# Kernel optimization log

Hardware: AMD Instinct MI355X
Metric: run time of the kernel (lower is better)

The kernel has to match this reference:

```python
import jax, jax.numpy as jnp
import numpy as np

N = 25600   # total nodes
B = 256     # graphs / batch_size / LSTM seq length
F = 128     # num_feat
H = 256     # gnn_hidden
R = 512     # rnn_hidden == 2*H (forced by alm layer)
L = 2       # rnn_layers
V = 32000   # vocab
E = 409600  # edges
NPG = 100   # nodes per graph (forced by alm layer / attention reshape)


def setup_inputs() -> dict:
    key = jax.random.key(0)
    ks = jax.random.split(key, 20)
    def rn(k, shape, fan_in, scale=1.0):
        return jax.random.normal(k, shape, jnp.float32) * (scale / np.sqrt(fan_in))
    inp = {}
    inp['x'] = jax.random.normal(ks[0], (N, F), jnp.float32)
    inp['edge_index'] = jax.random.randint(ks[1], (2, E), 0, N)
    inp['bwd_edge_index'] = jnp.flip(inp['edge_index'], axis=0)
    inp['batch'] = jnp.arange(N) // NPG  # contiguous graphs, 100 nodes each
    inp['h0'] = jax.random.normal(ks[2], (L, 1, R), jnp.float32)
    inp['c0'] = jax.random.normal(ks[3], (L, 1, R), jnp.float32)
    inp['W_gnn'] = rn(ks[4], (F, H), F)
    inp['W_root'] = rn(ks[5], (H, H), H)
    inp['W_nbr'] = rn(ks[6], (H, H), H)
    inp['b_conv'] = jnp.zeros((H,), jnp.float32)
    D = 2 * H
    inp['W1'] = rn(ks[7], (D, D), D); inp['b1'] = jnp.zeros((D,), jnp.float32)
    inp['gamma'] = jnp.ones((D,), jnp.float32); inp['beta'] = jnp.zeros((D,), jnp.float32)
    inp['W2'] = rn(ks[8], (D, D), D); inp['b2'] = jnp.zeros((D,), jnp.float32)
    A = NPG * R + R  # alm input dim = rnn_hidden*100 + rnn_hidden
    inp['W_alm'] = rn(ks[9], (NPG, A), A, scale=0.1)
    inp['b_alm'] = jnp.ones((NPG,), jnp.float32)  # keeps alpha.sum() well away from 0
    inp['Wih0'] = rn(ks[10], (4 * R, D), D); inp['Whh0'] = rn(ks[11], (4 * R, R), R)
    inp['bih0'] = jnp.zeros((4 * R,), jnp.float32); inp['bhh0'] = jnp.zeros((4 * R,), jnp.float32)
    inp['Wih1'] = rn(ks[12], (4 * R, R), R); inp['Whh1'] = rn(ks[13], (4 * R, R), R)
    inp['bih1'] = jnp.zeros((4 * R,), jnp.float32); inp['bhh1'] = jnp.zeros((4 * R,), jnp.float32)
    inp['W_fc'] = rn(ks[14], (R, V), R); inp['b_fc'] = jnp.zeros((V,), jnp.float32)
    return inp


def _lstm_layer(inputs, h, c, Wih, Whh, bih, bhh):
    # inputs: (T, 1, in); carry h, c: (1, R). PyTorch gate order i, f, g, o.
    def step(carry, xt):
        h, c = carry
        g = xt @ Wih.T + bih + h @ Whh.T + bhh
        i, f, gg, o = jnp.split(g, 4, axis=-1)
        c = jax.nn.sigmoid(f) * c + jax.nn.sigmoid(i) * jnp.tanh(gg)
        h = jax.nn.sigmoid(o) * jnp.tanh(c)
        return (h, c), h
    (hT, cT), outs = jax.lax.scan(step, (h, c), inputs)
    return outs, hT, cT


def reference(x, edge_index, bwd_edge_index, batch, h0, c0, W_gnn, W_root, W_nbr, b_conv,
              W1, b1, gamma, beta, W2, b2, W_alm, b_alm,
              Wih0, Whh0, bih0, bhh0, Wih1, Whh1, bih1, bhh1, W_fc, b_fc):
    n = x.shape[0]
    x = x @ W_gnn  # (N, H)
    # GraphConv: out_i = W_root x_i + W_nbr * sum_{j->i} x_j + b.
    # (Original loops gnn_layers times from the SAME x, so only the last conv matters.)
    def conv(xx, ei):
        agg = jax.ops.segment_sum(xx[ei[0]], ei[1], num_segments=n)
        return xx @ W_root + agg @ W_nbr + b_conv
    fwd_x = jax.nn.relu(conv(x, edge_index))
    bwd_x = jax.nn.relu(conv(x, bwd_edge_index))
    xc = jnp.concatenate([fwd_x, bwd_x], axis=1)  # (N, 2H) == (N, R)
    # MLP [2H, 2H, 2H]: Lin -> BatchNorm(batch stats) -> ReLU -> (dropout off) -> Lin
    h1 = xc @ W1 + b1
    h1 = (h1 - h1.mean(0)) / jnp.sqrt(h1.var(0) + 1e-5) * gamma + beta
    x_mlp = jax.nn.relu(h1) @ W2 + b2
    # global mean pool over graphs
    counts = jax.ops.segment_sum(jnp.ones((n,), x_mlp.dtype), batch, num_segments=B)
    x_g = jax.ops.segment_sum(x_mlp, batch, num_segments=B) / counts[:, None]
    x_emb = x_g.reshape(B, 1, 2 * H)  # LSTM: seq_len=B, batch=1
    # attention over cell state (vectorized form of the nested loops):
    # alpha[l,b,:] = alm(cat(c0[l].flatten(), h3[b].flatten())); normalize by sum (NOT softmax);
    # new_c[l] = sum_b alpha[l,b,:] @ h3[b]
    h3 = xc.reshape(B, NPG, R)
    s = c0.reshape(L, R)
    Ws, Wh = W_alm[:, :R], W_alm[:, R:]
    alpha = (s @ Ws.T)[:, None, :] + (h3.reshape(B, NPG * R) @ Wh.T)[None] + b_alm  # (L,B,NPG)
    alpha = alpha / alpha.sum(-1, keepdims=True)
    new_c = jnp.einsum('lbk,bkd->ld', alpha, h3)  # (L, R)
    # 2-layer LSTM (eval mode: inter-layer dropout is identity)
    outs, hT0, cT0 = _lstm_layer(x_emb, h0[0], new_c[0:1], Wih0, Whh0, bih0, bhh0)
    outs, hT1, cT1 = _lstm_layer(outs, h0[1], new_c[1:2], Wih1, Whh1, bih1, bhh1)
    preds = (outs @ W_fc + b_fc)[:, -1, :]  # (B, V)
    return preds
```

## Files before the change

kernel.cpp:

```cpp
#include <hip/hip_runtime.h>
#include <math.h>

#define N_NODES 25600
#define F_IN    128
#define H_GNN   256
#define D_MLP   512
#define E_EDGE  409600
#define B_GR    256
#define NPG_    100
#define R_LSTM  512
#define V_OUT   32000

typedef __bf16 bf16x8 __attribute__((ext_vector_type(8)));
typedef float  f32x4  __attribute__((ext_vector_type(4)));
typedef unsigned short u16x8 __attribute__((ext_vector_type(8)));

__device__ __forceinline__ unsigned short f2bf(float x) {
    unsigned u = __builtin_bit_cast(unsigned, x);
    unsigned r = (u + 0x7FFFu + ((u >> 16) & 1u)) >> 16;
    return (unsigned short)r;
}

template<bool TRANSB>
__global__ __launch_bounds__(256)
void gemm_tile(const float* __restrict__ A, const float* __restrict__ B,
               float* __restrict__ C, const float* __restrict__ bias,
               int M, int N, int K, int lda, int ldb, int ldc, int kChunk)
{
    __shared__ float As[16][68];
    __shared__ float Bs[16][68];
    const int tid = threadIdx.x;
    const int n0 = blockIdx.x * 64;
    const int m0 = blockIdx.y * 64;
    const int z  = blockIdx.z;
    const int k0 = z * kChunk;
    const int k1 = min(K, k0 + kChunk);
    const int ty = tid >> 4, tx = tid & 15;
    float acc[4][4] = {};

    for (int kb = k0; kb < k1; kb += 16) {
        {
            const int r = tid >> 4, c = tid & 15;
            #pragma unroll
            for (int i = 0; i < 4; ++i) {
                int rr = r + i * 16;
                int gm = m0 + rr, gk = kb + c;
                As[c][rr] = (gm < M && gk < k1) ? A[gm * lda + gk] : 0.f;
            }
        }
        if (!TRANSB) {
            const int r = tid >> 6, c = tid & 63;
            #pragma unroll
            for (int i = 0; i < 4; ++i) {
                int rr = r + i * 4;
                int gk = kb + rr, gn = n0 + c;
                Bs[rr][c] = (gk < k1 && gn < N) ? B[gk * ldb + gn] : 0.f;
            }
        } else {
            const int r = tid & 15, c = tid >> 4;
            #pragma unroll
            for (int i = 0; i < 4; ++i) {
                int cc = c + i * 16;
                int gk = kb + r, gn = n0 + cc;
                Bs[r][cc] = (gk < k1 && gn < N) ? B[gn * ldb + gk] : 0.f;
            }
        }
        __syncthreads();
        #pragma unroll
        for (int kk = 0; kk < 16; ++kk) {
            float a[4], b[4];
            #pragma unroll
            for (int i = 0; i < 4; ++i) a[i] = As[kk][ty * 4 + i];
            #pragma unroll
            for (int j = 0; j < 4; ++j) b[j] = Bs[kk][tx * 4 + j];
            #pragma unroll
            for (int i = 0; i < 4; ++i)
                #pragma unroll
                for (int j = 0; j < 4; ++j)
                    acc[i][j] = fmaf(a[i], b[j], acc[i][j]);
        }
        __syncthreads();
    }

    const bool split = (gridDim.z > 1);
    #pragma unroll
    for (int i = 0; i < 4; ++i) {
        int gm = m0 + ty * 4 + i;
        if (gm >= M) continue;
        #pragma unroll
        for (int j = 0; j < 4; ++j) {
            int gn = n0 + tx * 4 + j;
            if (gn >= N) continue;
            float v = acc[i][j];
            if (bias != nullptr && z == 0) v += bias[gn];
            if (split) atomicAdd(&C[gm * ldc + gn], v);
            else       C[gm * ldc + gn] = v;
        }
    }
}

__global__ __launch_bounds__(256)
void gemm_f32_big(const float* __restrict__ A, const float* __restrict__ B,
                  float* __restrict__ C, const float* __restrict__ bias,
                  int M, int N, int K, int lda, int ldb, int ldc)
{
    __shared__ float As[8][128];
    __shared__ float Bs[8][128];
    const int tid = threadIdx.x;
    const int tx = tid & 15, ty = tid >> 4;
    const int n0 = blockIdx.x * 128, m0 = blockIdx.y * 128;
    float acc[8][8] = {};

    for (int kb = 0; kb < K; kb += 8) {
        {
            int r = tid >> 1, c = (tid & 1) * 4;
            float4 v = *(const float4*)(A + (long)(m0 + r) * lda + kb + c);
            As[c + 0][r] = v.x; As[c + 1][r] = v.y;
            As[c + 2][r] = v.z; As[c + 3][r] = v.w;
        }
        {
            int r = tid >> 5, c = (tid & 31) * 4;
            *(float4*)&Bs[r][c] = *(const float4*)(B + (long)(kb + r) * ldb + n0 + c);
        }
        __syncthreads();
        #pragma unroll
        for (int kk = 0; kk < 8; ++kk) {
            float a[8], b[8];
            *(float4*)&a[0] = *(const float4*)&As[kk][ty * 8];
            *(float4*)&a[4] = *(const float4*)&As[kk][ty * 8 + 4];
            *(float4*)&b[0] = *(const float4*)&Bs[kk][tx * 8];
            *(float4*)&b[4] = *(const float4*)&Bs[kk][tx * 8 + 4];
            #pragma unroll
            for (int i = 0; i < 8; ++i)
                #pragma unroll
                for (int j = 0; j < 8; ++j)
                    acc[i][j] = fmaf(a[i], b[j], acc[i][j]);
        }
        __syncthreads();
    }

    #pragma unroll
    for (int i = 0; i < 8; ++i) {
        int gm = m0 + ty * 8 + i;
        #pragma unroll
        for (int j = 0; j < 8; j += 4) {
            int gn = n0 + tx * 8 + j;
            float4 v = {acc[i][j], acc[i][j+1], acc[i][j+2], acc[i][j+3]};
            if (bias != nullptr) {
                v.x += bias[gn]; v.y += bias[gn + 1];
                v.z += bias[gn + 2]; v.w += bias[gn + 3];
            }
            *(float4*)(C + (long)gm * ldc + gn) = v;
        }
    }
}

__global__ __launch_bounds__(256)
void mfma_gemm(const unsigned short* __restrict__ A,
               const unsigned short* __restrict__ Bt,
               float* __restrict__ C, const float* __restrict__ bias,
               int M, int N, int K, int lda, int ldb, int ldc, int kChunk)
{
    __shared__ unsigned short As[128][40];
    __shared__ unsigned short Bs[128][40];
    const int tid  = threadIdx.x;
    const int lane = tid & 63;
    const int wv   = tid >> 6;
    const int wr   = wv >> 1, wc = wv & 1;
    const int n0 = blockIdx.x * 128;
    const int m0 = blockIdx.y * 128;
    const int z  = blockIdx.z;
    const int k0 = z * kChunk;
    const int k1 = min(K, k0 + kChunk);

    const int srow = tid >> 2;
    const int skoff = (tid & 3) * 8;

    f32x4 acc[4][4] = {};

    for (int kb = k0; kb < k1; kb += 32) {
        #pragma unroll
        for (int p = 0; p < 2; ++p) {
            int row = p * 64 + srow;
            u16x8 va = *(const u16x8*)(A + (long)(m0 + row) * lda + kb + skoff);
            *(u16x8*)&As[row][skoff] = va;
            int gb = n0 + row;
            u16x8 vb = {0, 0, 0, 0, 0, 0, 0, 0};
            if (gb < N) vb = *(const u16x8*)(Bt + (long)gb * ldb + kb + skoff);
            *(u16x8*)&Bs[row][skoff] = vb;
        }
        __syncthreads();
        bf16x8 af[4], bfr[4];
        #pragma unroll
        for (int fm = 0; fm < 4; ++fm)
            af[fm] = *(const bf16x8*)&As[wr * 64 + fm * 16 + (lane & 15)][(lane >> 4) * 8];
        #pragma unroll
        for (int fn = 0; fn < 4; ++fn)
            bfr[fn] = *(const bf16x8*)&Bs[wc * 64 + fn * 16 + (lane & 15)][(lane >> 4) * 8];
        #pragma unroll
        for (int fm = 0; fm < 4; ++fm)
            #pragma unroll
            for (int fn = 0; fn < 4; ++fn)
                acc[fm][fn] = __builtin_amdgcn_mfma_f32_16x16x32_bf16(
                    af[fm], bfr[fn], acc[fm][fn], 0, 0, 0);
        __syncthreads();
    }

    const bool split = (gridDim.z > 1);
    #pragma unroll
    for (int fm = 0; fm < 4; ++fm) {
        int row = m0 + wr * 64 + fm * 16 + ((lane >> 4) << 2);
        #pragma unroll
        for (int fn = 0; fn < 4; ++fn) {
            int col = n0 + wc * 64 + fn * 16 + (lane & 15);
            if (col >= N) continue;
            f32x4 v = acc[fm][fn];
            #pragma unroll
            for (int r = 0; r < 4; ++r) {
                float o = v[r];
                if (bias != nullptr && z == 0) o += bias[col];
                if (split) atomicAdd(&C[(long)(row + r) * ldc + col], o);
                else       C[(long)(row + r) * ldc + col] = o;
            }
        }
    }
}

__global__ void castbf(const float* __restrict__ in, unsigned short* __restrict__ out,
                       long n) {
    long stride = (long)gridDim.x * blockDim.x * 4;
    for (long j = ((long)blockIdx.x * blockDim.x + threadIdx.x) * 4; j < n; j += stride) {
        float4 v = *(const float4*)(in + j);
        ushort4 o;
        o.x = f2bf(v.x); o.y = f2bf(v.y); o.z = f2bf(v.z); o.w = f2bf(v.w);
        *(ushort4*)(out + j) = o;
    }
}
__global__ void cast_strided(const float* __restrict__ in, unsigned short* __restrict__ out,
                             int cols, long ldin, long off) {
    const int r = blockIdx.y;
    int c = (blockIdx.x * blockDim.x + threadIdx.x) * 4;
    if (c < cols) {
        float4 v = *(const float4*)(in + (long)r * ldin + off + c);
        ushort4 o;
        o.x = f2bf(v.x); o.y = f2bf(v.y); o.z = f2bf(v.z); o.w = f2bf(v.w);
        *(ushort4*)(out + (long)r * cols + c) = o;
    }
}
__global__ __launch_bounds__(256)
void transcast(const float* __restrict__ in, unsigned short* __restrict__ out,
               int R, int C) {
    __shared__ unsigned short t[64][72];
    const int c0 = blockIdx.x * 64, r0 = blockIdx.y * 64;
    const int tid = threadIdx.x;
    const int rr = tid >> 2, cg = (tid & 3) * 16;
    #pragma unroll
    for (int i = 0; i < 4; ++i) {
        float4 v = *(const float4*)(in + (long)(r0 + rr) * C + c0 + cg + i * 4);
        t[cg + i * 4 + 0][rr] = f2bf(v.x);
        t[cg + i * 4 + 1][rr] = f2bf(v.y);
        t[cg + i * 4 + 2][rr] = f2bf(v.z);
        t[cg + i * 4 + 3][rr] = f2bf(v.w);
    }
    __syncthreads();
    const int cc = tid >> 2, kg = (tid & 3) * 16;
    #pragma unroll
    for (int i = 0; i < 2; ++i) {
        u16x8 v = *(const u16x8*)&t[cc][kg + i * 8];
        *(u16x8*)(out + (long)(c0 + cc) * R + r0 + kg + i * 8) = v;
    }
}

__global__ void zero_f32(float* p, long n) {
    for (long i = (long)blockIdx.x * blockDim.x + threadIdx.x; i < n;
         i += (long)gridDim.x * blockDim.x) p[i] = 0.f;
}
__global__ void zero_i32(int* p, long n) {
    for (long i = (long)blockIdx.x * blockDim.x + threadIdx.x; i < n;
         i += (long)gridDim.x * blockDim.x) p[i] = 0;
}
__global__ void addvec_kernel(const float* a, const float* b, float* o, int n) {
    int i = blockIdx.x * blockDim.x + threadIdx.x;
    if (i < n) o[i] = a[i] + b[i];
}
__global__ void concat_bias(const float* __restrict__ b_conv, float* bc2) {
    int i = blockIdx.x * blockDim.x + threadIdx.x;
    if (i < 512) bc2[i] = (i < 256) ? b_conv[i] : 0.f;
}

__global__ void hist_kernel(const int* __restrict__ key, int* counts, int E) {
    int i = blockIdx.x * blockDim.x + threadIdx.x;
    if (i < E) atomicAdd(&counts[key[i]], 1);
}
__global__ __launch_bounds__(256)
void scan_chunk(const int* __restrict__ counts, int* __restrict__ rowptr,
                int* __restrict__ tops, int n) {
    __shared__ int buf[256];
    const int tid = threadIdx.x;
    int i = blockIdx.x * 256 + tid;
    int v = (i < n) ? counts[i] : 0;
    buf[tid] = v;
    __syncthreads();
    for (int off = 1; off < 256; off <<= 1) {
        int add = (tid >= off) ? buf[tid - off] : 0;
        __syncthreads();
        buf[tid] += add;
        __syncthreads();
    }
    if (i < n) rowptr[i + 1] = buf[tid];
    if (tid == 255) tops[blockIdx.x] = buf[255];
}
__global__ __launch_bounds__(128)
void scan_tops(int* tops, int nt) {
    __shared__ int b[128];
    int tid = threadIdx.x;
    int v = (tid < nt) ? tops[tid] : 0;
    b[tid] = v;
    __syncthreads();
    for (int off = 1; off < 128; off <<= 1) {
        int add = (tid >= off) ? b[tid - off] : 0;
        __syncthreads();
        b[tid] += add;
        __syncthreads();
    }
    if (tid < nt) tops[tid] = b[tid] - v;
}
__global__ void scan_fixup(const int* __restrict__ counts, int* __restrict__ rowptr,
                           int* __restrict__ cursor, const int* __restrict__ tops, int n) {
    int i = blockIdx.x * blockDim.x + threadIdx.x;
    if (i < n) {
        int r = rowptr[i + 1] + tops[i >> 8];
        rowptr[i + 1] = r;
        cursor[i] = r - counts[i];
        if (i == 0) rowptr[0] = 0;
    }
}
__global__ void scatter_kernel(const int* __restrict__ key, const int* __restrict__ val,
                               int* cursor, int* sorted, int E) {
    int i = blockIdx.x * blockDim.x + threadIdx.x;
    if (i < E) {
        int pos = atomicAdd(&cursor[key[i]], 1);
        sorted[pos] = val[i];
    }
}
__global__ __launch_bounds__(256)
void agg_conv_kernel(const float* __restrict__ xrn,
                     const int* __restrict__ rowptr, const int* __restrict__ sorted,
                     float* __restrict__ xc, int outOff) {
    const int n = blockIdx.x, tid = threadIdx.x;
    float acc = xrn[(long)n * 512 + tid];
    const int s = rowptr[n], e = rowptr[n + 1];
    for (int t = s; t < e; ++t)
        acc += xrn[(long)sorted[t] * 512 + 256 + tid];
    xc[(long)n * 512 + outOff + tid] = fmaxf(acc, 0.f);
}

__global__ __launch_bounds__(512)
void colstat_kernel(const float* __restrict__ h1, float* colsum, float* colsq) {
    const int c = threadIdx.x;
    const int r0 = blockIdx.x * 128;
    float s = 0.f, s2 = 0.f;
    for (int r = 0; r < 128; ++r) {
        float v = h1[(long)(r0 + r) * D_MLP + c];
        s += v; s2 += v * v;
    }
    atomicAdd(&colsum[c], s);
    atomicAdd(&colsq[c], s2);
}
__global__ void finalize_stats(const float* colsum, const float* colsq,
                               const float* gamma, const float* beta,
                               float* scalev, float* shiftv) {
    int c = threadIdx.x;
    float m  = colsum[c] * (1.f / N_NODES);
    float vr = colsq[c] * (1.f / N_NODES) - m * m;
    float g  = gamma[c] * rsqrtf(vr + 1e-5f);
    scalev[c] = g;
    shiftv[c] = beta[c] - m * g;
}
__global__ void norm_relu(float* h, const float* __restrict__ sc,
                          const float* __restrict__ sh, long n) {
    for (long i = (long)blockIdx.x * blockDim.x + threadIdx.x; i < n;
         i += (long)gridDim.x * blockDim.x) {
        int c = (int)(i & 511);
        h[i] = fmaxf(fmaf(h[i], sc[c], sh[c]), 0.f);
    }
}
__global__ __launch_bounds__(512)
void pool_kernel(const float* __restrict__ hrelu, float* P) {
    const int b = blockIdx.x, c = threadIdx.x;
    float s = 0.f;
    for (int i = 0; i < NPG_; ++i) s += hrelu[(long)(b * NPG_ + i) * D_MLP + c];
    P[b * D_MLP + c] = s * (1.f / NPG_);
}
__global__ void sw_kernel(const float* __restrict__ c0, const float* __restrict__ W_alm,
                          float* sW) {
    int i = blockIdx.x * blockDim.x + threadIdx.x;
    if (i < 2 * NPG_) {
        int l = i / NPG_, p = i % NPG_;
        float s = 0.f;
        for (int k = 0; k < R_LSTM; ++k) s += c0[l * R_LSTM + k] * W_alm[p * 51712 + k];
        sW[l * NPG_ + p] = s;
    }
}
__global__ __launch_bounds__(128)
void alpha_kernel(const float* __restrict__ sW, const float* __restrict__ hW,
                  const float* __restrict__ b_alm, float* __restrict__ alpha) {
    const int lb = blockIdx.x;
    const int l = lb >> 8, b = lb & 255;
    const int p = threadIdx.x;
    __shared__ float red[128];
    float v = 0.f;
    if (p < NPG_) v = sW[l * NPG_ + p] + hW[b * NPG_ + p] + b_alm[p];
    red[p] = v;
    __syncthreads();
    for (int s = 64; s > 0; s >>= 1) {
        if (p < s) red[p] += red[p + s];
        __syncthreads();
    }
    float inv = 1.f / red[0];
    if (p < NPG_) alpha[lb * NPG_ + p] = v * inv;
}
__global__ __launch_bounds__(512)
void newc_kernel(const float* __restrict__ alpha, const float* __restrict__ xc,
                 float* new_c) {
    const int l = blockIdx.y, chunk = blockIdx.x, c = threadIdx.x;
    const int r0 = chunk * 800;
    float acc = 0.f;
    for (int r = r0; r < r0 + 800; ++r)
        acc += alpha[l * N_NODES + r] * xc[(long)r * D_MLP + c];
    atomicAdd(&new_c[l * D_MLP + c], acc);
}

#define CANARY 0x7FC00000u
#define SPIN_MAX 20000

__device__ __forceinline__ unsigned coh_load_u(const unsigned* p) {
    return __hip_atomic_load(p, __ATOMIC_RELAXED, __HIP_MEMORY_SCOPE_AGENT);
}
__device__ __forceinline__ void coh_store_f(float* p, float v) {
    __hip_atomic_store(p, v, __ATOMIC_RELAXED, __HIP_MEMORY_SCOPE_AGENT);
}

__global__ void lstm_init_kernel(const float* __restrict__ h0,
                                 float* h0buf, float* h1buf) {
    int i = blockIdx.x * blockDim.x + threadIdx.x;
    if (i < 512) { h0buf[i] = h0[i]; h1buf[i] = h0[512 + i]; }
    for (int j = 512 + i; j < 257 * 512; j += gridDim.x * blockDim.x) {
        ((unsigned*)h0buf)[j] = CANARY;
        ((unsigned*)h1buf)[j] = CANARY;
    }
}

__global__ __launch_bounds__(512)
void lstm_kernel(const float* __restrict__ inp0, const float* __restrict__ Whh0,
                 const float* __restrict__ Wih1, const float* __restrict__ Whh1,
                 const float* __restrict__ b1s, const float* __restrict__ new_c,
                 float* h0buf, float* h1buf)
{
    const int tid  = threadIdx.x;
    const int lane = tid & 63;
    const int w    = tid >> 6;
    const int blk  = blockIdx.x;
    const int layer = blk >> 5;
    const int base  = (blk & 31) * 16;
    const int gate  = lane >> 4;
    const int hid   = lane & 15;
    const int rowg  = gate * 512 + base + hid;

    __shared__ float partial[2][8][64];

    if (layer == 0) {
        float wr[64];
        {
            const float4* wp = (const float4*)(Whh0 + (long)rowg * 512 + w * 64);
            #pragma unroll
            for (int i = 0; i < 16; ++i) {
                float4 v = wp[i];
                wr[4*i] = v.x; wr[4*i+1] = v.y; wr[4*i+2] = v.z; wr[4*i+3] = v.w;
            }
        }
        float c = (w == 0 && lane < 16) ? new_c[base + lane] : 0.f;
        const unsigned* src_u = (const unsigned*)h0buf + w * 64 + lane;
        for (int t = 0; t < 256; ++t) {
            float ipv = (w == 0) ? inp0[t * 2048 + rowg] : 0.f;
            unsigned hu; int guard = 0;
            for (;;) {
                hu = coh_load_u(src_u + t * 512);
                if (!__any(hu == CANARY)) break;
                if (++guard > SPIN_MAX) break;
                if (guard > 32) __builtin_amdgcn_s_sleep(1);
            }
            float hv = __uint_as_float(hu);
            float acc = 0.f;
            #pragma unroll
            for (int j = 0; j < 64; ++j)
                acc = fmaf(wr[j], __shfl(hv, j), acc);
            partial[t & 1][w][lane] = acc;
            __syncthreads();
            if (w == 0) {
                float g = ipv;
                #pragma unroll
                for (int ww = 0; ww < 8; ++ww) g += partial[t & 1][ww][lane];
                float a = (gate == 2) ? tanhf(g) : 1.f / (1.f + expf(-g));
                float fv = __shfl(a, lane + 16);
                float gv = __shfl(a, lane + 32);
                float ov = __shfl(a, lane + 48);
                if (lane < 16) {
                    c = fv * c + a * gv;
                    float h = ov * tanhf(c);
                    coh_store_f(h0buf + (t + 1) * 512 + base + lane, h);
                }
            }
        }
    } else {
        const float* Wsel = (w < 4) ? Wih1 : Whh1;
        const int koff = (w & 3) * 128;
        float wrA[64], wrB[64];
        {
            const float4* wp = (const float4*)(Wsel + (long)rowg * 512 + koff);
            #pragma unroll
            for (int i = 0; i < 16; ++i) {
                float4 v = wp[i];
                wrA[4*i] = v.x; wrA[4*i+1] = v.y; wrA[4*i+2] = v.z; wrA[4*i+3] = v.w;
            }
            #pragma unroll
            for (int i = 0; i < 16; ++i) {
                float4 v = wp[16 + i];
                wrB[4*i] = v.x; wrB[4*i+1] = v.y; wrB[4*i+2] = v.z; wrB[4*i+3] = v.w;
            }
        }
        float bsum = (w == 0) ? b1s[rowg] : 0.f;
        float c = (w == 0 && lane < 16) ? new_c[512 + base + lane] : 0.f;
        for (int t = 0; t < 256; ++t) {
            const unsigned* xsrc = (w < 4)
                ? (const unsigned*)h0buf + (t + 1) * 512 + koff
                : (const unsigned*)h1buf + t * 512 + koff;
            unsigned hu0, hu1; int guard = 0;
            for (;;) {
                hu0 = coh_load_u(xsrc + lane);
                hu1 = coh_load_u(xsrc + 64 + lane);
                if (!__any((hu0 == CANARY) || (hu1 == CANARY))) break;
                if (++guard > SPIN_MAX) break;
                if (guard > 32) __builtin_amdgcn_s_sleep(1);
            }
            float hv0 = __uint_as_float(hu0), hv1 = __uint_as_float(hu1);
            float acc = 0.f;
            #pragma unroll
            for (int j = 0; j < 64; ++j)
                acc = fmaf(wrA[j], __shfl(hv0, j), acc);
            #pragma unroll
            for (int j = 0; j < 64; ++j)
                acc = fmaf(wrB[j], __shfl(hv1, j), acc);
            partial[t & 1][w][lane] = acc;
            __syncthreads();
            if (w == 0) {
                float g = bsum;
                #pragma unroll
                for (int ww = 0; ww < 8; ++ww) g += partial[t & 1][ww][lane];
                float a = (gate == 2) ? tanhf(g) : 1.f / (1.f + expf(-g));
                float fv = __shfl(a, lane + 16);
                float gv = __shfl(a, lane + 32);
                float ov = __shfl(a, lane + 48);
                if (lane < 16) {
                    c = fv * c + a * gv;
                    float h = ov * tanhf(c);
                    coh_store_f(h1buf + (t + 1) * 512 + base + lane, h);
                }
            }
        }
    }
}

extern "C" void kernel_launch(void* const* d_in, const int* in_sizes, int n_in,
                              void* d_out, int out_size, void* d_ws, size_t ws_size,
                              hipStream_t stream)
{
    const float* x      = (const float*)d_in[0];
    const int*   ei     = (const int*)d_in[1];
    const float* h0     = (const float*)d_in[4];
    const float* c0     = (const float*)d_in[5];
    const float* W_gnn  = (const float*)d_in[6];
    const float* W_root = (const float*)d_in[7];
    const float* W_nbr  = (const float*)d_in[8];
    const float* b_conv = (const float*)d_in[9];
    const float* W1     = (const float*)d_in[10];
    const float* b1     = (const float*)d_in[11];
    const float* gamma  = (const float*)d_in[12];
    const float* beta   = (const float*)d_in[13];
    const float* W2     = (const float*)d_in[14];
    const float* b2     = (const float*)d_in[15];
    const float* W_alm  = (const float*)d_in[16];
    const float* b_alm  = (const float*)d_in[17];
    const float* Wih0   = (const float*)d_in[18];
    const float* Whh0   = (const float*)d_in[19];
    const float* bih0   = (const float*)d_in[20];
    const float* bhh0   = (const float*)d_in[21];
    const float* Wih1   = (const float*)d_in[22];
    const float* Whh1   = (const float*)d_in[23];
    const float* bih1   = (const float*)d_in[24];
    const float* bhh1   = (const float*)d_in[25];
    const float* W_fc   = (const float*)d_in[26];
    const float* b_fc   = (const float*)d_in[27];
    float* out = (float*)d_out;
    float* ws  = (float*)d_ws;

    const int* ei0 = ei;
    const int* ei1 = ei + E_EDGE;

    float* xrn = ws;
    float* h1m = ws;
    unsigned short* Wfct  = (unsigned short*)ws;
    unsigned short* Walmb = (unsigned short*)(ws + 8500000L);
    unsigned short* ob    = (unsigned short*)(ws + 11200000L);
    float* xc = ws + 13107200L;
    long o = 26214400L;
    float* Wc    = ws + o; o += 65536;
    int*   counts= (int*)(ws + o); o += 25600;
    int*   rowptr= (int*)(ws + o); o += 25601;
    int*   cursor= (int*)(ws + o); o += 25600;
    int*   sorted= (int*)(ws + o); o += 409600;
    int*   tops  = (int*)(ws + o); o += 128;
    float* colsum= ws + o; o += 512;
    float* colsq = ws + o; o += 512;
    float* scalev= ws + o; o += 512;
    float* shiftv= ws + o; o += 512;
    float* P     = ws + o; o += 131072;
    float* x_g   = ws + o; o += 131072;
    float* hW    = ws + o; o += 25600;
    float* sW    = ws + o; o += 200;
    float* alphav= ws + o; o += 51200;
    float* newc  = ws + o; o += 1024;
    float* b0s   = ws + o; o += 2048;
    float* b1s   = ws + o; o += 2048;
    float* bc2   = ws + o; o += 512;
    unsigned short* xcb = (unsigned short*)(ws + o);
    float* inp0  = ws + o;
    float* h0st  = ws + o + 524288;
    float* h1st  = ws + o + 655872;
    o += 6553600;

    gemm_tile<false><<<dim3(4, 2, 1), 256, 0, stream>>>(W_gnn, W_root, Wc, nullptr,
        128, 256, 256, 256, 256, 512, 256);
    gemm_tile<false><<<dim3(4, 2, 1), 256, 0, stream>>>(W_gnn, W_nbr, Wc + 256, nullptr,
        128, 256, 256, 256, 256, 512, 256);
    concat_bias<<<dim3(2), 256, 0, stream>>>(b_conv, bc2);
    gemm_f32_big<<<dim3(4, 200), 256, 0, stream>>>(x, Wc, xrn, bc2,
        N_NODES, 512, 128, 128, 512, 512);
    zero_i32<<<dim3(100), 256, 0, stream>>>(counts, 25600);
    hist_kernel<<<dim3(1600), 256, 0, stream>>>(ei1, counts, E_EDGE);
    scan_chunk<<<dim3(100), 256, 0, stream>>>(counts, rowptr, tops, 25600);
    scan_tops<<<dim3(1), 128, 0, stream>>>(tops, 100);
    scan_fixup<<<dim3(100), 256, 0, stream>>>(counts, rowptr, cursor, tops, 25600);
    scatter_kernel<<<dim3(1600), 256, 0, stream>>>(ei1, ei0, cursor, sorted, E_EDGE);
    agg_conv_kernel<<<dim3(25600), 256, 0, stream>>>(xrn, rowptr, sorted, xc, 0);
    zero_i32<<<dim3(100), 256, 0, stream>>>(counts, 25600);
    hist_kernel<<<dim3(1600), 256, 0, stream>>>(ei0, counts, E_EDGE);
    scan_chunk<<<dim3(100), 256, 0, stream>>>(counts, rowptr, tops, 25600);
    scan_tops<<<dim3(1), 128, 0, stream>>>(tops, 100);
    scan_fixup<<<dim3(100), 256, 0, stream>>>(counts, rowptr, cursor, tops, 25600);
    scatter_kernel<<<dim3(1600), 256, 0, stream>>>(ei0, ei1, cursor, sorted, E_EDGE);
    agg_conv_kernel<<<dim3(25600), 256, 0, stream>>>(xrn, rowptr, sorted, xc, 256);
    gemm_f32_big<<<dim3(4, 200), 256, 0, stream>>>(xc, W1, h1m, b1,
        N_NODES, 512, 512, 512, 512, 512);
    zero_f32<<<dim3(4), 256, 0, stream>>>(colsum, 1024);
    colstat_kernel<<<dim3(200), 512, 0, stream>>>(h1m, colsum, colsq);
    finalize_stats<<<dim3(1), 512, 0, stream>>>(colsum, colsq, gamma, beta, scalev, shiftv);
    norm_relu<<<dim3(2048), 256, 0, stream>>>(h1m, scalev, shiftv, (long)N_NODES * 512);
    pool_kernel<<<dim3(256), 512, 0, stream>>>(h1m, P);
    gemm_tile<false><<<dim3(8, 4, 1), 256, 0, stream>>>(P, W2, x_g, b2,
        256, 512, 512, 512, 512, 512, 512);
    transcast<<<dim3(500, 8), 256, 0, stream>>>(W_fc, Wfct, 512, V_OUT);
    cast_strided<<<dim3(50, 100), 256, 0, stream>>>(W_alm, Walmb, 51200, 51712L, 512L);
    castbf<<<dim3(1024), 256, 0, stream>>>(xc, xcb, 13107200L);
    zero_f32<<<dim3(25), 256, 0, stream>>>(hW, 25600);
    mfma_gemm<<<dim3(1, 2, 32), 256, 0, stream>>>(xcb, Walmb, hW, nullptr,
        256, 100, 51200, 51200, 51200, 100, 1600);
    sw_kernel<<<dim3(1), 256, 0, stream>>>(c0, W_alm, sW);
    alpha_kernel<<<dim3(512), 128, 0, stream>>>(sW, hW, b_alm, alphav);
    zero_f32<<<dim3(1), 256, 0, stream>>>(newc, 1024);
    newc_kernel<<<dim3(32, 2), 512, 0, stream>>>(alphav, xc, newc);
    addvec_kernel<<<dim3(8), 256, 0, stream>>>(bih0, bhh0, b0s, 2048);
    addvec_kernel<<<dim3(8), 256, 0, stream>>>(bih1, bhh1, b1s, 2048);
    gemm_tile<true><<<dim3(32, 4, 1), 256, 0, stream>>>(x_g, Wih0, inp0, b0s,
        256, 2048, 512, 512, 512, 2048, 512);
    lstm_init_kernel<<<dim3(64), 512, 0, stream>>>(h0, h0st, h1st);
    lstm_kernel<<<dim3(64), 512, 0, stream>>>(inp0, Whh0, Wih1, Whh1, b1s, newc,
                                              h0st, h1st);
    castbf<<<dim3(128), 256, 0, stream>>>(h1st + 512, ob, 131072L);
    mfma_gemm<<<dim3(250, 2, 1), 256, 0, stream>>>(ob, Wfct, out, b_fc,
        256, V_OUT, 512, 512, 512, V_OUT, 512);
}
```

Baseline: 1.868 ms.

## Fuse preprocessing, CSR builds, aggregation, bf16 cast and norm-pool kernels; widen split-K

Folds the small bias, zeroing and sW kernels into one prep kernel. Builds the forward and backward CSR structures together in paired hist, scan and scatter kernels. A single 512-thread aggregation kernel now handles both directions and writes the bf16 copy of xc, which removes the separate castbf pass. BatchNorm-apply+ReLU is fused into mean pooling so the full h1 rewrite is skipped, and the hW split-K GEMM goes from 32 to 100 K-chunks. Together these cut launch count and memory traffic, at the cost of more atomic contention on hW and combined atomic traffic in hist/scatter.

```diff
diff --git a/kernel.cpp b/kernel.cpp
--- a/kernel.cpp
+++ b/kernel.cpp
@@ -271,33 +271,61 @@
     }
 }
 
-__global__ void zero_f32(float* p, long n) {
-    for (long i = (long)blockIdx.x * blockDim.x + threadIdx.x; i < n;
-         i += (long)gridDim.x * blockDim.x) p[i] = 0.f;
-}
 __global__ void zero_i32(int* p, long n) {
     for (long i = (long)blockIdx.x * blockDim.x + threadIdx.x; i < n;
          i += (long)gridDim.x * blockDim.x) p[i] = 0;
 }
-__global__ void addvec_kernel(const float* a, const float* b, float* o, int n) {
+__global__ __launch_bounds__(256)
+void prep_kernel(const float* __restrict__ bih0, const float* __restrict__ bhh0,
+                 const float* __restrict__ bih1, const float* __restrict__ bhh1,
+                 const float* __restrict__ b_conv, const float* __restrict__ c0,
+                 const float* __restrict__ W_alm,
+                 float* b0s, float* b1s, float* bc2, float* sW,
+                 float* colsum, float* colsq, float* newc, float* hW) {
+    const int b = blockIdx.x, t = threadIdx.x;
+    if (b < 8) {
+        int i = b * 256 + t;
+        b0s[i] = bih0[i] + bhh0[i];
+        b1s[i] = bih1[i] + bhh1[i];
+    } else if (b == 8) {
+        bc2[t] = b_conv[t];
+        bc2[t + 256] = 0.f;
+    } else if (b == 9) {
+        if (t < 2 * NPG_) {
+            int l = t / NPG_, p = t % NPG_;
+            float s = 0.f;
+            for (int k = 0; k < R_LSTM; ++k)
+                s += c0[l * R_LSTM + k] * W_alm[(long)p * 51712 + k];
+            sW[l * NPG_ + p] = s;
+        }
+    } else if (b == 10) {
+        for (int i = t; i < 512; i += 256) { colsum[i] = 0.f; colsq[i] = 0.f; }
+        for (int i = t; i < 1024; i += 256) newc[i] = 0.f;
+    } else {
+        int i = (b - 11) * 256 + t;
+        if (i < 25600) hW[i] = 0.f;
+    }
+}
+
+__global__ void hist2_kernel(const int* __restrict__ ei0, const int* __restrict__ ei1,
+                             int* counts_d, int* counts_s, int E) {
     int i = blockIdx.x * blockDim.x + threadIdx.x;
-    if (i < n) o[i] = a[i] + b[i];
-}
-__global__ void concat_bias(const float* __restrict__ b_conv, float* bc2) {
-    int i = blockIdx.x * blockDim.x + threadIdx.x;
-    if (i < 512) bc2[i] = (i < 256) ? b_conv[i] : 0.f;
-}
-
-__global__ void hist_kernel(const int* __restrict__ key, int* counts, int E) {
-    int i = blockIdx.x * blockDim.x + threadIdx.x;
-    if (i < E) atomicAdd(&counts[key[i]], 1);
+    if (i < E) {
+        atomicAdd(&counts_d[ei1[i]], 1);
+        atomicAdd(&counts_s[ei0[i]], 1);
+    }
 }
 __global__ __launch_bounds__(256)
-void scan_chunk(const int* __restrict__ counts, int* __restrict__ rowptr,
-                int* __restrict__ tops, int n) {
+void scan_chunk2(const int* __restrict__ counts_d, const int* __restrict__ counts_s,
+                 int* rowptr_d, int* rowptr_s, int* tops_d, int* tops_s, int n) {
     __shared__ int buf[256];
+    const int half = blockIdx.x >= 100;
+    const int chunk = half ? blockIdx.x - 100 : blockIdx.x;
+    const int* counts = half ? counts_s : counts_d;
+    int* rowptr = half ? rowptr_s : rowptr_d;
+    int* tops   = half ? tops_s   : tops_d;
     const int tid = threadIdx.x;
-    int i = blockIdx.x * 256 + tid;
+    int i = chunk * 256 + tid;
     int v = (i < n) ? counts[i] : 0;
     buf[tid] = v;
     __syncthreads();
@@ -308,11 +336,12 @@
         __syncthreads();
     }
     if (i < n) rowptr[i + 1] = buf[tid];
-    if (tid == 255) tops[blockIdx.x] = buf[255];
+    if (tid == 255) tops[chunk] = buf[255];
 }
 __global__ __launch_bounds__(128)
-void scan_tops(int* tops, int nt) {
+void scan_tops2(int* tops_d, int* tops_s, int nt) {
     __shared__ int b[128];
+    int* tops = (blockIdx.x == 0) ? tops_d : tops_s;
     int tid = threadIdx.x;
     int v = (tid < nt) ? tops[tid] : 0;
     b[tid] = v;
@@ -325,34 +354,56 @@
     }
     if (tid < nt) tops[tid] = b[tid] - v;
 }
-__global__ void scan_fixup(const int* __restrict__ counts, int* __restrict__ rowptr,
-                           int* __restrict__ cursor, const int* __restrict__ tops, int n) {
-    int i = blockIdx.x * blockDim.x + threadIdx.x;
+__global__ void scan_fixup2(const int* __restrict__ counts_d, const int* __restrict__ counts_s,
+                            int* rowptr_d, int* rowptr_s,
+                            int* cursor_d, int* cursor_s,
+                            const int* __restrict__ tops_d, const int* __restrict__ tops_s,
+                            int n) {
+    const int half = blockIdx.x >= 100;
+    const int chunk = half ? blockIdx.x - 100 : blockIdx.x;
+    const int* counts = half ? counts_s : counts_d;
+    const int* tops   = half ? tops_s   : tops_d;
+    int* rowptr = half ? rowptr_s : rowptr_d;
+    int* cursor = half ? cursor_s : cursor_d;
+    int i = chunk * 256 + threadIdx.x;
     if (i < n) {
-        int r = rowptr[i + 1] + tops[i >> 8];
+        int r = rowptr[i + 1] + tops[chunk];
         rowptr[i + 1] = r;
         cursor[i] = r - counts[i];
         if (i == 0) rowptr[0] = 0;
     }
 }
-__global__ void scatter_kernel(const int* __restrict__ key, const int* __restrict__ val,
-                               int* cursor, int* sorted, int E) {
+__global__ void scatter2_kernel(const int* __restrict__ ei0, const int* __restrict__ ei1,
+                                int* cursor_d, int* cursor_s,
+                                int* sorted_d, int* sorted_s, int E) {
     int i = blockIdx.x * blockDim.x + threadIdx.x;
     if (i < E) {
-        int pos = atomicAdd(&cursor[key[i]], 1);
-        sorted[pos] = val[i];
-    }
-}
-__global__ __launch_bounds__(256)
-void agg_conv_kernel(const float* __restrict__ xrn,
-                     const int* __restrict__ rowptr, const int* __restrict__ sorted,
-                     float* __restrict__ xc, int outOff) {
-    const int n = blockIdx.x, tid = threadIdx.x;
-    float acc = xrn[(long)n * 512 + tid];
+        int s = ei0[i], d = ei1[i];
+        int pd = atomicAdd(&cursor_d[d], 1);
+        sorted_d[pd] = s;
+        int ps = atomicAdd(&cursor_s[s], 1);
+        sorted_s[ps] = d;
+    }
+}
+__global__ __launch_bounds__(512)
+void agg_conv2(const float* __restrict__ xrn,
+               const int* __restrict__ rowptr_d, const int* __restrict__ sorted_d,
+               const int* __restrict__ rowptr_s, const int* __restrict__ sorted_s,
+               float* __restrict__ xc, unsigned short* __restrict__ xcb) {
+    const int n = blockIdx.x;
+    const int tid = threadIdx.x;
+    const int c = tid & 255;
+    const bool bwd = tid >= 256;
+    const int* rowptr = bwd ? rowptr_s : rowptr_d;
+    const int* sorted = bwd ? sorted_s : sorted_d;
+    float acc = xrn[(long)n * 512 + c];
     const int s = rowptr[n], e = rowptr[n + 1];
     for (int t = s; t < e; ++t)
-        acc += xrn[(long)sorted[t] * 512 + 256 + tid];
-    xc[(long)n * 512 + outOff + tid] = fmaxf(acc, 0.f);
+        acc += xrn[(long)sorted[t] * 512 + 256 + c];
+    float r = fmaxf(acc, 0.f);
+    long idx = (long)n * 512 + (bwd ? 256 : 0) + c;
+    xc[idx] = r;
+    xcb[idx] = f2bf(r);
 }
 
 __global__ __launch_bounds__(512)
@@ -377,30 +428,17 @@
     scalev[c] = g;
     shiftv[c] = beta[c] - m * g;
 }
-__global__ void norm_relu(float* h, const float* __restrict__ sc,
-                          const float* __restrict__ sh, long n) {
-    for (long i = (long)blockIdx.x * blockDim.x + threadIdx.x; i < n;
-         i += (long)gridDim.x * blockDim.x) {
-        int c = (int)(i & 511);
-        h[i] = fmaxf(fmaf(h[i], sc[c], sh[c]), 0.f);
-    }
-}
 __global__ __launch_bounds__(512)
-void pool_kernel(const float* __restrict__ hrelu, float* P) {
+void fused_norm_pool(const float* __restrict__ h1, const float* __restrict__ sc,
+                     const float* __restrict__ sh, float* __restrict__ P) {
     const int b = blockIdx.x, c = threadIdx.x;
+    const float scv = sc[c], shv = sh[c];
     float s = 0.f;
-    for (int i = 0; i < NPG_; ++i) s += hrelu[(long)(b * NPG_ + i) * D_MLP + c];
+    for (int i = 0; i < NPG_; ++i) {
+        float v = h1[(long)(b * NPG_ + i) * D_MLP + c];
+        s += fmaxf(fmaf(v, scv, shv), 0.f);
+    }
     P[b * D_MLP + c] = s * (1.f / NPG_);
-}
-__global__ void sw_kernel(const float* __restrict__ c0, const float* __restrict__ W_alm,
-                          float* sW) {
-    int i = blockIdx.x * blockDim.x + threadIdx.x;
-    if (i < 2 * NPG_) {
-        int l = i / NPG_, p = i % NPG_;
-        float s = 0.f;
-        for (int k = 0; k < R_LSTM; ++k) s += c0[l * R_LSTM + k] * W_alm[p * 51712 + k];
-        sW[l * NPG_ + p] = s;
-    }
 }
 __global__ __launch_bounds__(128)
 void alpha_kernel(const float* __restrict__ sW, const float* __restrict__ hW,
@@ -480,12 +518,12 @@
             }
         }
         float c = (w == 0 && lane < 16) ? new_c[base + lane] : 0.f;
-        const unsigned* src_u = (const unsigned*)h0buf + w * 64 + lane;
+        const unsigned* src = (const unsigned*)h0buf + w * 64 + lane;
         for (int t = 0; t < 256; ++t) {
             float ipv = (w == 0) ? inp0[t * 2048 + rowg] : 0.f;
             unsigned hu; int guard = 0;
             for (;;) {
-                hu = coh_load_u(src_u + t * 512);
+                hu = coh_load_u(src + (long)t * 512);
                 if (!__any(hu == CANARY)) break;
                 if (++guard > SPIN_MAX) break;
                 if (guard > 32) __builtin_amdgcn_s_sleep(1);
@@ -508,7 +546,7 @@
                 if (lane < 16) {
                     c = fv * c + a * gv;
                     float h = ov * tanhf(c);
-                    coh_store_f(h0buf + (t + 1) * 512 + base + lane, h);
+                    coh_store_f(h0buf + (long)(t + 1) * 512 + base + lane, h);
                 }
             }
         }
@@ -533,8 +571,8 @@
         float c = (w == 0 && lane < 16) ? new_c[512 + base + lane] : 0.f;
         for (int t = 0; t < 256; ++t) {
             const unsigned* xsrc = (w < 4)
-                ? (const unsigned*)h0buf + (t + 1) * 512 + koff
-                : (const unsigned*)h1buf + t * 512 + koff;
+                ? (const unsigned*)h0buf + (long)(t + 1) * 512 + koff
+                : (const unsigned*)h1buf + (long)t * 512 + koff;
             unsigned hu0, hu1; int guard = 0;
             for (;;) {
                 hu0 = coh_load_u(xsrc + lane);
@@ -564,7 +602,7 @@
                 if (lane < 16) {
                     c = fv * c + a * gv;
                     float h = ov * tanhf(c);
-                    coh_store_f(h1buf + (t + 1) * 512 + base + lane, h);
+                    coh_store_f(h1buf + (long)(t + 1) * 512 + base + lane, h);
                 }
             }
         }
@@ -615,11 +653,16 @@
     float* xc = ws + 13107200L;
     long o = 26214400L;
     float* Wc    = ws + o; o += 65536;
-    int*   counts= (int*)(ws + o); o += 25600;
-    int*   rowptr= (int*)(ws + o); o += 25601;
-    int*   cursor= (int*)(ws + o); o += 25600;
-    int*   sorted= (int*)(ws + o); o += 409600;
-    int*   tops  = (int*)(ws + o); o += 128;
+    int*   counts_d = (int*)(ws + o); o += 25600;
+    int*   counts_s = (int*)(ws + o); o += 25600;
+    int*   rowptr_d = (int*)(ws + o); o += 25601;
+    int*   rowptr_s = (int*)(ws + o); o += 25601;
+    int*   cursor_d = (int*)(ws + o); o += 25600;
+    int*   cursor_s = (int*)(ws + o); o += 25600;
+    int*   sorted_d = (int*)(ws + o); o += 409600;
+    int*   sorted_s = (int*)(ws + o); o += 409600;
+    int*   tops_d   = (int*)(ws + o); o += 128;
+    int*   tops_s   = (int*)(ws + o); o += 128;
     float* colsum= ws + o; o += 512;
     float* colsq = ws + o; o += 512;
     float* scalev= ws + o; o += 512;
@@ -639,48 +682,39 @@
     float* h1st  = ws + o + 655872;
     o += 6553600;
 
+    prep_kernel<<<dim3(111), 256, 0, stream>>>(bih0, bhh0, bih1, bhh1, b_conv, c0,
+                                               W_alm, b0s, b1s, bc2, sW,
+                                               colsum, colsq, newc, hW);
     gemm_tile<false><<<dim3(4, 2, 1), 256, 0, stream>>>(W_gnn, W_root, Wc, nullptr,
         128, 256, 256, 256, 256, 512, 256);
     gemm_tile<false><<<dim3(4, 2, 1), 256, 0, stream>>>(W_gnn, W_nbr, Wc + 256, nullptr,
         128, 256, 256, 256, 256, 512, 256);
-    concat_bias<<<dim3(2), 256, 0, stream>>>(b_conv, bc2);
     gemm_f32_big<<<dim3(4, 200), 256, 0, stream>>>(x, Wc, xrn, bc2,
         N_NODES, 512, 128, 128, 512, 512);
-    zero_i32<<<dim3(100), 256, 0, stream>>>(counts, 25600);
-    hist_kernel<<<dim3(1600), 256, 0, stream>>>(ei1, counts, E_EDGE);
-    scan_chunk<<<dim3(100), 256, 0, stream>>>(counts, rowptr, tops, 25600);
-    scan_tops<<<dim3(1), 128, 0, stream>>>(tops, 100);
-    scan_fixup<<<dim3(100), 256, 0, stream>>>(counts, rowptr, cursor, tops, 25600);
-    scatter_kernel<<<dim3(1600), 256, 0, stream>>>(ei1, ei0, cursor, sorted, E_EDGE);
-    agg_conv_kernel<<<dim3(25600), 256, 0, stream>>>(xrn, rowptr, sorted, xc, 0);
-    zero_i32<<<dim3(100), 256, 0, stream>>>(counts, 25600);
-    hist_kernel<<<dim3(1600), 256, 0, stream>>>(ei0, counts, E_EDGE);
-    scan_chunk<<<dim3(100), 256, 0, stream>>>(counts, rowptr, tops, 25600);
-    scan_tops<<<dim3(1), 128, 0, stream>>>(tops, 100);
-    scan_fixup<<<dim3(100), 256, 0, stream>>>(counts, rowptr, cursor, tops, 25600);
-    scatter_kernel<<<dim3(1600), 256, 0, stream>>>(ei0, ei1, cursor, sorted, E_EDGE);
-    agg_conv_kernel<<<dim3(25600), 256, 0, stream>>>(xrn, rowptr, sorted, xc, 256);
+    zero_i32<<<dim3(200), 256, 0, stream>>>(counts_d, 51200);
+    hist2_kernel<<<dim3(1600), 256, 0, stream>>>(ei0, ei1, counts_d, counts_s, E_EDGE);
+    scan_chunk2<<<dim3(200), 256, 0, stream>>>(counts_d, counts_s, rowptr_d, rowptr_s,
+                                               tops_d, tops_s, 25600);
+    scan_tops2<<<dim3(2), 128, 0, stream>>>(tops_d, tops_s, 100);
+    scan_fixup2<<<dim3(200), 256, 0, stream>>>(counts_d, counts_s, rowptr_d, rowptr_s,
+                                               cursor_d, cursor_s, tops_d, tops_s, 25600);
+    scatter2_kernel<<<dim3(1600), 256, 0, stream>>>(ei0, ei1, cursor_d, cursor_s,
+                                                    sorted_d, sorted_s, E_EDGE);
+    agg_conv2<<<dim3(25600), 512, 0, stream>>>(xrn, rowptr_d, sorted_d,
+                                               rowptr_s, sorted_s, xc, xcb);
     gemm_f32_big<<<dim3(4, 200), 256, 0, stream>>>(xc, W1, h1m, b1,
         N_NODES, 512, 512, 512, 512, 512);
-    zero_f32<<<dim3(4), 256, 0, stream>>>(colsum, 1024);
     colstat_kernel<<<dim3(200), 512, 0, stream>>>(h1m, colsum, colsq);
     finalize_stats<<<dim3(1), 512, 0, stream>>>(colsum, colsq, gamma, beta, scalev, shiftv);
-    norm_relu<<<dim3(2048), 256, 0, stream>>>(h1m, scalev, shiftv, (long)N_NODES * 512);
-    pool_kernel<<<dim3(256), 512, 0, stream>>>(h1m, P);
+    fused_norm_pool<<<dim3(256), 512, 0, stream>>>(h1m, scalev, shiftv, P);
     gemm_tile<false><<<dim3(8, 4, 1), 256, 0, stream>>>(P, W2, x_g, b2,
         256, 512, 512, 512, 512, 512, 512);
     transcast<<<dim3(500, 8), 256, 0, stream>>>(W_fc, Wfct, 512, V_OUT);
     cast_strided<<<dim3(50, 100), 256, 0, stream>>>(W_alm, Walmb, 51200, 51712L, 512L);
-    castbf<<<dim3(1024), 256, 0, stream>>>(xc, xcb, 13107200L);
-    zero_f32<<<dim3(25), 256, 0, stream>>>(hW, 25600);
-    mfma_gemm<<<dim3(1, 2, 32), 256, 0, stream>>>(xcb, Walmb, hW, nullptr,
-        256, 100, 51200, 51200, 51200, 100, 1600);
-    sw_kernel<<<dim3(1), 256, 0, stream>>>(c0, W_alm, sW);
+    mfma_gemm<<<dim3(1, 2, 100), 256, 0, stream>>>(xcb, Walmb, hW, nullptr,
+        256, 100, 51200, 51200, 51200, 100, 512);
     alpha_kernel<<<dim3(512), 128, 0, stream>>>(sW, hW, b_alm, alphav);
-    zero_f32<<<dim3(1), 256, 0, stream>>>(newc, 1024);
     newc_kernel<<<dim3(32, 2), 512, 0, stream>>>(alphav, xc, newc);
-    addvec_kernel<<<dim3(8), 256, 0, stream>>>(bih0, bhh0, b0s, 2048);
-    addvec_kernel<<<dim3(8), 256, 0, stream>>>(bih1, bhh1, b1s, 2048);
     gemm_tile<true><<<dim3(32, 4, 1), 256, 0, stream>>>(x_g, Wih0, inp0, b0s,
         256, 2048, 512, 512, 512, 2048, 512);
     lstm_init_kernel<<<dim3(64), 512, 0, stream>>>(h0, h0st, h1st);
```

After: 1.894 ms. About the same (+1.4%).
